# Kernel optimization log

Hardware: AMD Instinct MI355X
Metric: run time of the kernel (lower is better)

Reference implementation:

```python
import jax, jax.numpy as jnp
import numpy as np

D = 4096  # uniform layer width (sizes[i])
L = 4     # number of MyLinear layers (maximum)


def setup_inputs() -> dict:
    key = jax.random.key(0)
    ks = jax.random.split(key, 8)
    x = jax.random.normal(ks[0], (D,), jnp.float32)
    W_in = jax.random.normal(ks[1], (D, D), jnp.float32) / np.float32(np.sqrt(D))
    b_in = jax.random.normal(ks[2], (D,), jnp.float32) * 0.01
    weights = jax.random.normal(ks[3], (L, D, D), jnp.float32) / np.float32(np.sqrt(D))
    # `order` is a fixed 0/1-style connectivity mask (requires_grad=False in torch)
    orders = (jax.random.uniform(ks[4], (L, D, D)) < 0.5).astype(jnp.float32)
    biases = jax.random.normal(ks[5], (L, D), jnp.float32) * 0.01
    # input_layer[i]: which node slots feed layer i (irregular gather)
    gather_idx = jax.random.randint(ks[6], (L, D), 0, D)
    # layer_nodes[k]: where layer outputs are scattered (per-layer permutation)
    scatter_idx = jnp.stack(
        [jax.random.permutation(jax.random.fold_in(ks[7], i), D) for i in range(L + 1)]
    )
    return dict(x=x, W_in=W_in, b_in=b_in, weights=weights, orders=orders,
                biases=biases, gather_idx=gather_idx, scatter_idx=scatter_idx)


def reference(x, W_in, b_in, weights, orders, biases, gather_idx, scatter_idx):
    # input layer: relu(Linear(x)), scattered into the node buffer
    out0 = jax.nn.relu(W_in @ x + b_in)              # [D]
    buf = jnp.zeros_like(out0).at[scatter_idx[0]].set(out0)

    def step(buf, layer):
        W, O, b, g, s = layer
        inp = buf[g]                                  # gather node values [D]
        out = jax.nn.relu((W * O) @ inp + b)          # masked GEMV + bias + relu
        new_buf = jnp.zeros_like(out).at[s].set(out)  # scatter into node buffer
        return new_buf, out

    _, outs = jax.lax.scan(
        step, buf, (weights, orders, biases, gather_idx, scatter_idx[1:])
    )
    return outs[-1]  # forward returns the last layer's (pre-scatter) output
```

## Files before the change

kernel.cpp:

```cpp
#include <hip/hip_runtime.h>
#include <hip/hip_bf16.h>


#define DD 4096
#define BLOCK 1024
#define GRID  256

template<bool MASKED>
__global__ __launch_bounds__(BLOCK, 4)
void gemv_kernel(const float* __restrict__ W,
                 const float* __restrict__ O,
                 const float* __restrict__ bias,
                 const float* __restrict__ src,
                 const int*   __restrict__ g,
                 const int*   __restrict__ s,
                 float*       __restrict__ dst)
{
    __shared__ float sh[DD];
    const int tid  = threadIdx.x;
    const int lane = tid & 63;
    const int wv   = tid >> 6;
    const int row  = blockIdx.x * 16 + wv;

    const float* __restrict__ Wr = W + (size_t)row * DD + lane * 4;
    const float* __restrict__ Or = MASKED ? (O + (size_t)row * DD + lane * 4)
                                          : nullptr;

    float4 wb[8], ob[8];
    #pragma unroll
    for (int k = 0; k < 8; ++k) {
        wb[k] = *reinterpret_cast<const float4*>(Wr + k * 256);
        if (MASKED) ob[k] = *reinterpret_cast<const float4*>(Or + k * 256);
    }

    #pragma unroll
    for (int j = tid; j < DD; j += BLOCK)
        sh[j] = MASKED ? src[g[j]] : src[j];
    __syncthreads();

    float a0 = 0.f, a1 = 0.f, a2 = 0.f, a3 = 0.f;
    #pragma unroll
    for (int it = 0; it < 16; ++it) {
        float4 v = *reinterpret_cast<const float4*>(sh + it * 256 + lane * 4);
        float4 w = wb[it & 7];
        float4 o;
        if (MASKED) o = ob[it & 7];
        if (it < 8) {
            wb[it] = *reinterpret_cast<const float4*>(Wr + (it + 8) * 256);
            if (MASKED) ob[it] = *reinterpret_cast<const float4*>(Or + (it + 8) * 256);
        }
        if (MASKED) { w.x *= o.x; w.y *= o.y; w.z *= o.z; w.w *= o.w; }
        a0 = fmaf(w.x, v.x, a0);
        a1 = fmaf(w.y, v.y, a1);
        a2 = fmaf(w.z, v.z, a2);
        a3 = fmaf(w.w, v.w, a3);
    }
    float acc = (a0 + a1) + (a2 + a3);

    #pragma unroll
    for (int off = 32; off; off >>= 1) acc += __shfl_xor(acc, off, 64);

    if (lane == 0) {
        float r = fmaxf(acc + bias[row], 0.f);
        if (s) dst[s[row]] = r;
        else   dst[row]    = r;
    }
}

extern "C" void kernel_launch(void* const* d_in, const int* in_sizes, int n_in,
                              void* d_out, int out_size, void* d_ws, size_t ws_size,
                              hipStream_t stream) {
    const float* x       = (const float*)d_in[0];
    const float* W_in    = (const float*)d_in[1];
    const float* b_in    = (const float*)d_in[2];
    const float* weights = (const float*)d_in[3];
    const float* orders  = (const float*)d_in[4];
    const float* biases  = (const float*)d_in[5];
    const int*   gidx    = (const int*)d_in[6];
    const int*   sidx    = (const int*)d_in[7];
    float*       out     = (float*)d_out;

    float* buf0 = (float*)d_ws;
    float* buf1 = buf0 + DD;

    gemv_kernel<false><<<GRID, BLOCK, 0, stream>>>(
        W_in, nullptr, b_in, x, nullptr, sidx, buf0);

    float* cur = buf0;
    float* nxt = buf1;
    for (int l = 0; l < 4; ++l) {
        const int* s  = (l == 3) ? nullptr : (sidx + (size_t)(l + 1) * DD);
        float*     d  = (l == 3) ? out     : nxt;
        gemv_kernel<true><<<GRID, BLOCK, 0, stream>>>(
            weights + (size_t)l * DD * DD,
            orders  + (size_t)l * DD * DD,
            biases  + (size_t)l * DD,
            cur, gidx + (size_t)l * DD, s, d);
        float* t = cur; cur = nxt; nxt = t;
    }
}
```

Before: 548.5 us.

## Restructure GEMV so each wave covers a column slice across sixteen rows

Each wave now computes partial dot products over a 256-column slice for all 16 rows of the block, instead of one full row per wave. The gathered input vector slice is loaded once per thread, and partials are reduced via wave shuffles and a shared-memory table. This drops the manual double-buffered prefetch of weights and adds many more shuffle reductions plus an extra barrier.

```diff
diff --git a/kernel.cpp b/kernel.cpp
--- a/kernel.cpp
+++ b/kernel.cpp
@@ -5,6 +5,7 @@
 #define DD 4096
 #define BLOCK 1024
 #define GRID  256
+#define RPB   16
 
 template<bool MASKED>
 __global__ __launch_bounds__(BLOCK, 4)
@@ -17,53 +18,53 @@
                  float*       __restrict__ dst)
 {
     __shared__ float sh[DD];
+    __shared__ float partial[RPB][RPB + 1];
     const int tid  = threadIdx.x;
     const int lane = tid & 63;
     const int wv   = tid >> 6;
-    const int row  = blockIdx.x * 16 + wv;
-
-    const float* __restrict__ Wr = W + (size_t)row * DD + lane * 4;
-    const float* __restrict__ Or = MASKED ? (O + (size_t)row * DD + lane * 4)
-                                          : nullptr;
-
-    float4 wb[8], ob[8];
-    #pragma unroll
-    for (int k = 0; k < 8; ++k) {
-        wb[k] = *reinterpret_cast<const float4*>(Wr + k * 256);
-        if (MASKED) ob[k] = *reinterpret_cast<const float4*>(Or + k * 256);
-    }
+    const int row0 = blockIdx.x * RPB;
 
     #pragma unroll
     for (int j = tid; j < DD; j += BLOCK)
         sh[j] = MASKED ? src[g[j]] : src[j];
     __syncthreads();
 
-    float a0 = 0.f, a1 = 0.f, a2 = 0.f, a3 = 0.f;
+    const int col = wv * 256 + lane * 4;
+    const float4 v = *reinterpret_cast<const float4*>(sh + col);
+
+    const float* __restrict__ Wp = W + (size_t)row0 * DD + col;
+    const float* __restrict__ Op = MASKED ? (O + (size_t)row0 * DD + col)
+                                          : nullptr;
+
+    float acc[RPB];
     #pragma unroll
-    for (int it = 0; it < 16; ++it) {
-        float4 v = *reinterpret_cast<const float4*>(sh + it * 256 + lane * 4);
-        float4 w = wb[it & 7];
-        float4 o;
-        if (MASKED) o = ob[it & 7];
-        if (it < 8) {
-            wb[it] = *reinterpret_cast<const float4*>(Wr + (it + 8) * 256);
-            if (MASKED) ob[it] = *reinterpret_cast<const float4*>(Or + (it + 8) * 256);
+    for (int r = 0; r < RPB; ++r) {
+        float4 w = *reinterpret_cast<const float4*>(Wp + (size_t)r * DD);
+        if (MASKED) {
+            float4 o = *reinterpret_cast<const float4*>(Op + (size_t)r * DD);
+            w.x *= o.x; w.y *= o.y; w.z *= o.z; w.w *= o.w;
         }
-        if (MASKED) { w.x *= o.x; w.y *= o.y; w.z *= o.z; w.w *= o.w; }
-        a0 = fmaf(w.x, v.x, a0);
-        a1 = fmaf(w.y, v.y, a1);
-        a2 = fmaf(w.z, v.z, a2);
-        a3 = fmaf(w.w, v.w, a3);
+        acc[r] = fmaf(w.x, v.x, fmaf(w.y, v.y, fmaf(w.z, v.z, w.w * v.w)));
     }
-    float acc = (a0 + a1) + (a2 + a3);
 
     #pragma unroll
-    for (int off = 32; off; off >>= 1) acc += __shfl_xor(acc, off, 64);
+    for (int r = 0; r < RPB; ++r) {
+        float a = acc[r];
+        #pragma unroll
+        for (int off = 32; off; off >>= 1)
+            a += __shfl_xor(a, off, 64);
+        if (lane == 0) partial[r][wv] = a;
+    }
+    __syncthreads();
 
-    if (lane == 0) {
-        float r = fmaxf(acc + bias[row], 0.f);
-        if (s) dst[s[row]] = r;
-        else   dst[row]    = r;
+    if (tid < RPB) {
+        const int r = row0 + tid;
+        float t = 0.f;
+        #pragma unroll
+        for (int w2 = 0; w2 < RPB; ++w2) t += partial[tid][w2];
+        t = fmaxf(t + bias[r], 0.f);
+        if (s) dst[s[r]] = t;
+        else   dst[r]    = t;
     }
 }
 
```

Result: slower. 597.7 us (+9.0%).
